# Performance work log

Measured on AMD Instinct MI355X. Metric: run time of the kernel, lower is better.

Reference implementation:

```python
import jax, jax.numpy as jnp
import numpy as np

D_MODEL = 512
NUM_HEADS = 8
HEAD_DIM = D_MODEL // NUM_HEADS  # 64
B, L = 8, 1024


def setup_inputs() -> dict:
    key = jax.random.key(0)
    ks = jax.random.split(key, 6)
    scale = 1.0 / np.sqrt(D_MODEL)
    return {
        "x": jax.random.normal(ks[0], (B, L, D_MODEL), dtype=jnp.float32),
        "mask": jax.random.normal(ks[1], (L, L), dtype=jnp.float32),
        "Wqkv": jax.random.normal(ks[2], (D_MODEL, 3 * D_MODEL), dtype=jnp.float32) * scale,
        "bqkv": jax.random.normal(ks[3], (3 * D_MODEL,), dtype=jnp.float32) * 0.01,
        "Wo": jax.random.normal(ks[4], (D_MODEL, D_MODEL), dtype=jnp.float32) * scale,
        "bo": jax.random.normal(ks[5], (D_MODEL,), dtype=jnp.float32) * 0.01,
    }


def reference(x, mask, Wqkv, bqkv, Wo, bo):
    b, l, _ = x.shape
    qkv = x @ Wqkv + bqkv                                   # [B, L, 3*D]
    # Faithful to torch: reshape to [B, L, H, 3*head_dim] then chunk last dim.
    qkv = qkv.reshape(b, l, NUM_HEADS, 3 * HEAD_DIM)
    qkv = jnp.transpose(qkv, (0, 2, 1, 3))                  # [B, H, L, 3*hd]
    q, k, v = jnp.split(qkv, 3, axis=-1)                    # each [B, H, L, hd]
    scaled = jnp.einsum("bhqd,bhkd->bhqk", q, k) / np.sqrt(HEAD_DIM)
    scaled = scaled + mask                                  # mask broadcasts over [B, H]
    attn = jax.nn.softmax(scaled, axis=-1)
    out = jnp.einsum("bhqk,bhkd->bhqd", attn, v)            # [B, H, L, hd]
    out = jnp.transpose(out, (0, 2, 1, 3)).reshape(b, l, D_MODEL)
    return out @ Wo + bo
```

## Files before the change

### kernel.cpp

```cpp
#include <hip/hip_runtime.h>
#include <hip/hip_bf16.h>
#include <stdint.h>

#define B_ 8
#define L_ 1024
#define DM 512
#define H_ 8
#define HD 64
#define N3 1536
#define M_T (B_*L_)
#define LOG2E 1.44269504f

typedef __attribute__((ext_vector_type(8))) short short8;
typedef __attribute__((ext_vector_type(4))) float f32x4;
typedef __attribute__((ext_vector_type(4))) float float4_t;
typedef __attribute__((ext_vector_type(4))) unsigned short ushort4_t;

#define MFMA16(a,b,c) __builtin_amdgcn_mfma_f32_16x16x32_bf16((a),(b),(c),0,0,0)

__device__ __forceinline__ short f2bf(float f){
  union { float f; unsigned u; } v; v.f = f;
  unsigned r = v.u + 0x7fffu + ((v.u >> 16) & 1u);
  return (short)(r >> 16);
}

__device__ __forceinline__ short f2bf_fast(float f){
  __hip_bfloat16 h = __float2bfloat16(f);
  short s; __builtin_memcpy(&s, &h, 2); return s;
}

__global__ __launch_bounds__(256) void k_cvt(const float* __restrict__ x,
                                             short* __restrict__ xb, int n8){
  int i = blockIdx.x*256 + threadIdx.x;
  if (i >= n8) return;
  const float4_t* p = (const float4_t*)x + (size_t)i*2;
  float4_t a = p[0], b = p[1];
  short8 o;
  o[0]=f2bf(a[0]); o[1]=f2bf(a[1]); o[2]=f2bf(a[2]); o[3]=f2bf(a[3]);
  o[4]=f2bf(b[0]); o[5]=f2bf(b[1]); o[6]=f2bf(b[2]); o[7]=f2bf(b[3]);
  *((short8*)xb + i) = o;
}

__global__ __launch_bounds__(256) void k_tr2(const float* __restrict__ W0, short* __restrict__ WT0,
                                             const float* __restrict__ W1, short* __restrict__ WT1){
  __shared__ float t[64][65];
  const float* W; short* WT; int N, n0;
  if (blockIdx.x < 24){ W = W0; WT = WT0; N = N3; n0 = blockIdx.x*64; }
  else                { W = W1; WT = WT1; N = DM; n0 = (blockIdx.x-24)*64; }
  int k0 = blockIdx.y*64;
  int tid = threadIdx.x;
  int r = tid >> 4, c4 = (tid & 15) * 4;
  #pragma unroll
  for (int it=0; it<4; ++it){
    int rr = r + it*16;
    float4_t v = *(const float4_t*)(W + (size_t)(k0+rr)*N + n0 + c4);
    t[rr][c4+0]=v[0]; t[rr][c4+1]=v[1]; t[rr][c4+2]=v[2]; t[rr][c4+3]=v[3];
  }
  __syncthreads();
  #pragma unroll
  for (int it=0; it<4; ++it){
    int n = r + it*16;
    ushort4_t o;
    o[0]=(unsigned short)f2bf(t[c4+0][n]);
    o[1]=(unsigned short)f2bf(t[c4+1][n]);
    o[2]=(unsigned short)f2bf(t[c4+2][n]);
    o[3]=(unsigned short)f2bf(t[c4+3][n]);
    *(ushort4_t*)(WT + (size_t)(n0+n)*DM + k0 + c4) = o;
  }
}

__global__ __launch_bounds__(256) void k_maskp(const float* __restrict__ mask,
                                               float* __restrict__ maskP){
  int gid = blockIdx.x*256 + threadIdx.x;
  int nf  = gid & 3;
  int lane= (gid>>2) & 63;
  int kvt = (gid>>8) & 15;
  int qg  = gid>>12;
  int li = lane & 15, lg = lane >> 4;
  int r0 = qg*16 + lg*4;
  int col = kvt*64 + nf*16 + li;
  float4_t o;
  #pragma unroll
  for (int j=0;j<4;++j)
    o[j] = fmaf(mask[(size_t)(r0+j)*1024 + col], LOG2E, -17.3123405f);
  ((float4_t*)maskP)[gid] = o;
}

__global__ __launch_bounds__(256) void k_gemm_qkv(
    const short* __restrict__ A, const short* __restrict__ Bt,
    const float* __restrict__ bias,
    short* __restrict__ Qo, short* __restrict__ Ko, short* __restrict__ VTo)
{
  __shared__ __align__(16) short As[2][128*40];
  __shared__ __align__(16) short Bs[2][128*40];
  const int m0 = blockIdx.x*128, n0 = blockIdx.y*128;
  const int tid = threadIdx.x;
  const int w = tid>>6, lane = tid&63, li = lane&15, lg = lane>>4;
  const int wr = (w>>1)*64, wc = (w&1)*64;

  int row[2], seg[2];
  #pragma unroll
  for (int c=0;c<2;++c){ int s = tid + c*256; row[c]=s>>2; seg[c]=s&3; }

  short8 ga[2], gb[2];
  #pragma unroll
  for (int c=0;c<2;++c){
    ga[c] = *(const short8*)(A  + (size_t)(m0+row[c])*DM + seg[c]*8);
    gb[c] = *(const short8*)(Bt + (size_t)(n0+row[c])*DM + seg[c]*8);
  }

  const f32x4 fz = {0.f,0.f,0.f,0.f};
  f32x4 acc[4][4];
  #pragma unroll
  for (int i=0;i<4;++i)
    #pragma unroll
    for (int j=0;j<4;++j) acc[i][j] = fz;

  for (int kt=0; kt<16; ++kt){
    short* as = As[kt&1]; short* bs = Bs[kt&1];
    #pragma unroll
    for (int c=0;c<2;++c){
      *(short8*)&as[row[c]*40 + seg[c]*8] = ga[c];
      *(short8*)&bs[row[c]*40 + seg[c]*8] = gb[c];
    }
    __syncthreads();
    if (kt < 15){
      int k0 = (kt+1)*32;
      #pragma unroll
      for (int c=0;c<2;++c){
        ga[c] = *(const short8*)(A  + (size_t)(m0+row[c])*DM + k0 + seg[c]*8);
        gb[c] = *(const short8*)(Bt + (size_t)(n0+row[c])*DM + k0 + seg[c]*8);
      }
    }
    short8 bfr[4];
    #pragma unroll
    for (int nf=0;nf<4;++nf)
      bfr[nf] = *(const short8*)&bs[(wc + nf*16 + li)*40 + lg*8];
    __builtin_amdgcn_s_setprio(1);
    #pragma unroll
    for (int mf=0;mf<4;++mf){
      short8 af = *(const short8*)&as[(wr + mf*16 + li)*40 + lg*8];
      #pragma unroll
      for (int nf=0;nf<4;++nf)
        acc[mf][nf] = MFMA16(af, bfr[nf], acc[mf][nf]);
    }
    __builtin_amdgcn_s_setprio(0);
    __syncthreads();
  }

  #pragma unroll
  for (int nf=0;nf<4;++nf){
    int n = n0 + wc + nf*16 + li;
    float bv = bias[n];
    unsigned h  = (unsigned)n / 192u;
    unsigned wn = (unsigned)n % 192u;
    unsigned typ = wn >> 6, d = wn & 63u;
    #pragma unroll
    for (int mf=0;mf<4;++mf){
      #pragma unroll
      for (int j=0;j<4;++j){
        int m  = m0 + wr + mf*16 + lg*4 + j;
        int b  = m >> 10, lp = m & 1023;
        size_t bh = (size_t)(b*8 + (int)h);
        float vf = acc[mf][nf][j] + bv;
        if (typ == 0)      Qo [(bh<<16) + ((size_t)lp<<6)  + d]  = f2bf_fast(vf * 0.18033688f);
        else if (typ == 1) Ko [(bh<<16) + ((size_t)lp<<6)  + d]  = f2bf_fast(vf);
        else               VTo[(bh<<16) + ((size_t)d<<10)  + lp] = f2bf_fast(vf);
      }
    }
  }
}

__global__ __launch_bounds__(512) void k_attn(
    const short* __restrict__ Q, const short* __restrict__ Kb,
    const short* __restrict__ VT, const float* __restrict__ maskP,
    short* __restrict__ O2)
{
  __shared__ __align__(16) short Ks[2][64*72];
  __shared__ __align__(16) short Vs[2][64*72];
  __shared__ __align__(16) short Ps[8][16*72];
  const int bh = blockIdx.y;
  const int q0 = blockIdx.x*128;
  const int tid = threadIdx.x, w = tid>>6, lane = tid&63, li = lane&15, lg = lane>>4;
  const int qw = q0 + w*16;

  const short* Qp = Q  + ((size_t)bh<<16);
  const short* Kp = Kb + ((size_t)bh<<16);
  const short* Vp = VT + ((size_t)bh<<16);

  short8 qf[2];
  #pragma unroll
  for (int t=0;t<2;++t)
    qf[t] = *(const short8*)(Qp + ((size_t)(qw+li)<<6) + t*32 + lg*8);

  short8 ones8;
  #pragma unroll
  for (int e=0;e<8;++e) ones8[e] = (short)0x3f80;

  const f32x4 fz = {0.f,0.f,0.f,0.f};
  f32x4 o[4], osum = fz;
  #pragma unroll
  for (int df=0;df<4;++df) o[df] = fz;

  const int srow = tid>>3, sseg8 = (tid&7)*8;

  short8 gk = *(const short8*)(Kp + ((size_t)srow<<6) + sseg8);
  short8 gv = *(const short8*)(Vp + ((size_t)srow<<10) + sseg8);
  *(short8*)&Ks[0][srow*72 + sseg8] = gk;
  *(short8*)&Vs[0][srow*72 + sseg8] = gv;
  gk = *(const short8*)(Kp + ((size_t)(64+srow)<<6) + sseg8);
  gv = *(const short8*)(Vp + ((size_t)srow<<10) + 64 + sseg8);
  __syncthreads();

  const float* mp0 = maskP + ((size_t)(qw>>4)<<14) + lane*16;
  short* pw = Ps[w];

  for (int kvt=0; kvt<16; ++kvt){
    const short* ks = Ks[kvt&1];
    const short* vs = Vs[kvt&1];
    if (kvt < 15){
      short* kd = Ks[(kvt&1)^1]; short* vd = Vs[(kvt&1)^1];
      *(short8*)&kd[srow*72 + sseg8] = gk;
      *(short8*)&vd[srow*72 + sseg8] = gv;
    }
    if (kvt < 14){
      int nx = (kvt+2)*64;
      gk = *(const short8*)(Kp + ((size_t)(nx+srow)<<6) + sseg8);
      gv = *(const short8*)(Vp + ((size_t)srow<<10) + nx + sseg8);
    }

    const float* mp = mp0 + (size_t)kvt*1024;
    f32x4 s[4];
    #pragma unroll
    for (int nf=0;nf<4;++nf)
      s[nf] = *(const float4_t*)(mp + nf*4);

    __builtin_amdgcn_s_setprio(1);
    #pragma unroll
    for (int nf=0;nf<4;++nf){
      #pragma unroll
      for (int t=0;t<2;++t){
        short8 kf = *(const short8*)&ks[(nf*16+li)*72 + t*32 + lg*8];
        s[nf] = MFMA16(qf[t], kf, s[nf]);
      }
    }
    __builtin_amdgcn_s_setprio(0);

    #pragma unroll
    for (int nf=0;nf<4;++nf)
      #pragma unroll
      for (int j=0;j<4;++j)
        pw[(lg*4+j)*72 + nf*16 + li] = f2bf_fast(exp2f(s[nf][j]));

    __builtin_amdgcn_s_setprio(1);
    #pragma unroll
    for (int t=0;t<2;++t){
      short8 pf = *(const short8*)&pw[li*72 + t*32 + lg*8];
      osum = MFMA16(pf, ones8, osum);
      #pragma unroll
      for (int df=0;df<4;++df){
        short8 vf = *(const short8*)&vs[(df*16+li)*72 + t*32 + lg*8];
        o[df] = MFMA16(pf, vf, o[df]);
      }
    }
    __builtin_amdgcn_s_setprio(0);

    __syncthreads();
  }

  int b = bh >> 3, h = bh & 7;
  float rl[4];
  #pragma unroll
  for (int j=0;j<4;++j) rl[j] = 1.0f / osum[j];
  #pragma unroll
  for (int df=0;df<4;++df)
    #pragma unroll
    for (int j=0;j<4;++j){
      int m   = b*1024 + qw + lg*4 + j;
      int col = h*64 + df*16 + li;
      O2[(size_t)m*512 + col] = f2bf_fast(o[df][j] * rl[j]);
    }
}

__global__ __launch_bounds__(256) void k_gemm_out(
    const short* __restrict__ A, const short* __restrict__ Bt,
    const float* __restrict__ bias, float* __restrict__ out)
{
  __shared__ __align__(16) short As[2][128*40];
  __shared__ __align__(16) short Bs[2][128*40];
  const int m0 = blockIdx.x*128, n0 = blockIdx.y*128;
  const int tid = threadIdx.x;
  const int w = tid>>6, lane = tid&63, li = lane&15, lg = lane>>4;
  const int wr = (w>>1)*64, wc = (w&1)*64;

  int row[2], seg[2];
  #pragma unroll
  for (int c=0;c<2;++c){ int s = tid + c*256; row[c]=s>>2; seg[c]=s&3; }

  short8 ga[2], gb[2];
  #pragma unroll
  for (int c=0;c<2;++c){
    ga[c] = *(const short8*)(A  + (size_t)(m0+row[c])*DM + seg[c]*8);
    gb[c] = *(const short8*)(Bt + (size_t)(n0+row[c])*DM + seg[c]*8);
  }

  const f32x4 fz = {0.f,0.f,0.f,0.f};
  f32x4 acc[4][4];
  #pragma unroll
  for (int i=0;i<4;++i)
    #pragma unroll
    for (int j=0;j<4;++j) acc[i][j] = fz;

  for (int kt=0; kt<16; ++kt){
    short* as = As[kt&1]; short* bs = Bs[kt&1];
    #pragma unroll
    for (int c=0;c<2;++c){
      *(short8*)&as[row[c]*40 + seg[c]*8] = ga[c];
      *(short8*)&bs[row[c]*40 + seg[c]*8] = gb[c];
    }
    __syncthreads();
    if (kt < 15){
      int k0 = (kt+1)*32;
      #pragma unroll
      for (int c=0;c<2;++c){
        ga[c] = *(const short8*)(A  + (size_t)(m0+row[c])*DM + k0 + seg[c]*8);
        gb[c] = *(const short8*)(Bt + (size_t)(n0+row[c])*DM + k0 + seg[c]*8);
      }
    }
    short8 bfr[4];
    #pragma unroll
    for (int nf=0;nf<4;++nf)
      bfr[nf] = *(const short8*)&bs[(wc + nf*16 + li)*40 + lg*8];
    __builtin_amdgcn_s_setprio(1);
    #pragma unroll
    for (int mf=0;mf<4;++mf){
      short8 af = *(const short8*)&as[(wr + mf*16 + li)*40 + lg*8];
      #pragma unroll
      for (int nf=0;nf<4;++nf)
        acc[mf][nf] = MFMA16(af, bfr[nf], acc[mf][nf]);
    }
    __builtin_amdgcn_s_setprio(0);
    __syncthreads();
  }

  #pragma unroll
  for (int nf=0;nf<4;++nf){
    int n = n0 + wc + nf*16 + li;
    float bv = bias[n];
    #pragma unroll
    for (int mf=0;mf<4;++mf){
      #pragma unroll
      for (int j=0;j<4;++j){
        int m = m0 + wr + mf*16 + lg*4 + j;
        out[(size_t)m*DM + n] = acc[mf][nf][j] + bv;
      }
    }
  }
}

extern "C" void kernel_launch(void* const* d_in, const int* in_sizes, int n_in,
                              void* d_out, int out_size, void* d_ws, size_t ws_size,
                              hipStream_t stream)
{
  (void)in_sizes; (void)n_in; (void)out_size; (void)ws_size;
  const float* x    = (const float*)d_in[0];
  const float* mask = (const float*)d_in[1];
  const float* Wqkv = (const float*)d_in[2];
  const float* bqkv = (const float*)d_in[3];
  const float* Wo   = (const float*)d_in[4];
  const float* bo   = (const float*)d_in[5];
  float* out = (float*)d_out;

  short* xb    = (short*)d_ws;
  short* WqkvT = xb    + (size_t)M_T*DM;
  short* WoT   = WqkvT + (size_t)N3*DM;
  short* Qb    = WoT   + (size_t)DM*DM;
  short* Kbf   = Qb    + (size_t)64*1024*64;
  short* VTb   = Kbf   + (size_t)64*1024*64;
  short* O2    = VTb   + (size_t)64*1024*64;
  float* maskP = (float*)xb;

  k_cvt<<<2048, 256, 0, stream>>>(x, xb, (M_T*DM)/8);
  k_tr2<<<dim3(32, 8), 256, 0, stream>>>(Wqkv, WqkvT, Wo, WoT);
  k_gemm_qkv<<<dim3(M_T/128, N3/128), 256, 0, stream>>>(xb, WqkvT, bqkv, Qb, Kbf, VTb);
  k_maskp<<<1024, 256, 0, stream>>>(mask, maskP);
  k_attn    <<<dim3(L_/128, B_*H_),   512, 0, stream>>>(Qb, Kbf, VTb, maskP, O2);
  k_gemm_out<<<dim3(M_T/128, DM/128), 256, 0, stream>>>(O2, WoT, bo, out);
}
```

Baseline: 93.76 us.

## Give each attention wave two query row-blocks, transpose score layout, prefetch mask

The attention kernel drops from 512 to 256 threads per block, and each wave now handles 32 query rows instead of 16. Each K and V fragment read from shared memory then feeds twice as many MFMAs. The QK^T product is computed transposed (K as the A operand), so the mask permutation and the P stores change layout, and P is packed with v_cvt_pk_bf16_f32 into wider stores. The next tile's mask is prefetched into registers, and the accumulator is seeded directly with the mask. The cost is higher register pressure and fewer waves per block, which could limit latency hiding.

```diff
diff --git a/kernel.cpp b/kernel.cpp
--- a/kernel.cpp
+++ b/kernel.cpp
@@ -15,6 +15,7 @@
 typedef __attribute__((ext_vector_type(4))) float f32x4;
 typedef __attribute__((ext_vector_type(4))) float float4_t;
 typedef __attribute__((ext_vector_type(4))) unsigned short ushort4_t;
+typedef __attribute__((ext_vector_type(2))) unsigned int u32x2;
 
 #define MFMA16(a,b,c) __builtin_amdgcn_mfma_f32_16x16x32_bf16((a),(b),(c),0,0,0)
 
@@ -77,12 +78,12 @@
   int kvt = (gid>>8) & 15;
   int qg  = gid>>12;
   int li = lane & 15, lg = lane >> 4;
-  int r0 = qg*16 + lg*4;
-  int col = kvt*64 + nf*16 + li;
+  int row = qg*16 + li;
+  int col = kvt*64 + nf*16 + lg*4;
+  float4_t m = *(const float4_t*)(mask + (size_t)row*1024 + col);
   float4_t o;
   #pragma unroll
-  for (int j=0;j<4;++j)
-    o[j] = fmaf(mask[(size_t)(r0+j)*1024 + col], LOG2E, -17.3123405f);
+  for (int j=0;j<4;++j) o[j] = fmaf(m[j], LOG2E, -17.3123405f);
   ((float4_t*)maskP)[gid] = o;
 }
 
@@ -171,48 +172,77 @@
   }
 }
 
-__global__ __launch_bounds__(512) void k_attn(
+__global__ __launch_bounds__(256, 2) void k_attn(
     const short* __restrict__ Q, const short* __restrict__ Kb,
     const short* __restrict__ VT, const float* __restrict__ maskP,
     short* __restrict__ O2)
 {
   __shared__ __align__(16) short Ks[2][64*72];
   __shared__ __align__(16) short Vs[2][64*72];
-  __shared__ __align__(16) short Ps[8][16*72];
+  __shared__ __align__(16) short Ps[4][32*72];
   const int bh = blockIdx.y;
   const int q0 = blockIdx.x*128;
   const int tid = threadIdx.x, w = tid>>6, lane = tid&63, li = lane&15, lg = lane>>4;
-  const int qw = q0 + w*16;
+  const int qw = q0 + w*32;
 
   const short* Qp = Q  + ((size_t)bh<<16);
   const short* Kp = Kb + ((size_t)bh<<16);
   const short* Vp = VT + ((size_t)bh<<16);
 
-  short8 qf[2];
-  #pragma unroll
-  for (int t=0;t<2;++t)
-    qf[t] = *(const short8*)(Qp + ((size_t)(qw+li)<<6) + t*32 + lg*8);
+  short8 qf[2][2];
+  #pragma unroll
+  for (int mb=0;mb<2;++mb)
+    #pragma unroll
+    for (int t=0;t<2;++t)
+      qf[mb][t] = *(const short8*)(Qp + ((size_t)(qw+mb*16+li)<<6) + t*32 + lg*8);
 
   short8 ones8;
   #pragma unroll
   for (int e=0;e<8;++e) ones8[e] = (short)0x3f80;
 
   const f32x4 fz = {0.f,0.f,0.f,0.f};
-  f32x4 o[4], osum = fz;
-  #pragma unroll
-  for (int df=0;df<4;++df) o[df] = fz;
-
-  const int srow = tid>>3, sseg8 = (tid&7)*8;
-
-  short8 gk = *(const short8*)(Kp + ((size_t)srow<<6) + sseg8);
-  short8 gv = *(const short8*)(Vp + ((size_t)srow<<10) + sseg8);
-  *(short8*)&Ks[0][srow*72 + sseg8] = gk;
-  *(short8*)&Vs[0][srow*72 + sseg8] = gv;
-  gk = *(const short8*)(Kp + ((size_t)(64+srow)<<6) + sseg8);
-  gv = *(const short8*)(Vp + ((size_t)srow<<10) + 64 + sseg8);
+  f32x4 o[2][4], osum[2];
+  #pragma unroll
+  for (int mb=0;mb<2;++mb){
+    osum[mb] = fz;
+    #pragma unroll
+    for (int df=0;df<4;++df) o[mb][df] = fz;
+  }
+
+  int srow[2], sseg[2];
+  #pragma unroll
+  for (int c=0;c<2;++c){ int f = tid + c*256; srow[c]=f>>3; sseg[c]=(f&7)*8; }
+
+  short8 gk[2], gv[2];
+  #pragma unroll
+  for (int c=0;c<2;++c){
+    gk[c] = *(const short8*)(Kp + ((size_t)srow[c]<<6)  + sseg[c]);
+    gv[c] = *(const short8*)(Vp + ((size_t)srow[c]<<10) + sseg[c]);
+  }
+  #pragma unroll
+  for (int c=0;c<2;++c){
+    *(short8*)&Ks[0][srow[c]*72 + sseg[c]] = gk[c];
+    *(short8*)&Vs[0][srow[c]*72 + sseg[c]] = gv[c];
+  }
+  #pragma unroll
+  for (int c=0;c<2;++c){
+    gk[c] = *(const short8*)(Kp + ((size_t)(64+srow[c])<<6) + sseg[c]);
+    gv[c] = *(const short8*)(Vp + ((size_t)srow[c]<<10) + 64 + sseg[c]);
+  }
+
+  const float* mpb[2];
+  #pragma unroll
+  for (int mb=0;mb<2;++mb)
+    mpb[mb] = maskP + ((size_t)((qw>>4)+mb)<<14) + lane*16;
+  f32x4 mnx[2][4];
+  #pragma unroll
+  for (int mb=0;mb<2;++mb)
+    #pragma unroll
+    for (int nf=0;nf<4;++nf)
+      mnx[mb][nf] = *(const float4_t*)(mpb[mb] + nf*4);
+
   __syncthreads();
 
-  const float* mp0 = maskP + ((size_t)(qw>>4)<<14) + lane*16;
   short* pw = Ps[w];
 
   for (int kvt=0; kvt<16; ++kvt){
@@ -220,47 +250,69 @@
     const short* vs = Vs[kvt&1];
     if (kvt < 15){
       short* kd = Ks[(kvt&1)^1]; short* vd = Vs[(kvt&1)^1];
-      *(short8*)&kd[srow*72 + sseg8] = gk;
-      *(short8*)&vd[srow*72 + sseg8] = gv;
+      #pragma unroll
+      for (int c=0;c<2;++c){
+        *(short8*)&kd[srow[c]*72 + sseg[c]] = gk[c];
+        *(short8*)&vd[srow[c]*72 + sseg[c]] = gv[c];
+      }
     }
     if (kvt < 14){
       int nx = (kvt+2)*64;
-      gk = *(const short8*)(Kp + ((size_t)(nx+srow)<<6) + sseg8);
-      gv = *(const short8*)(Vp + ((size_t)srow<<10) + nx + sseg8);
-    }
-
-    const float* mp = mp0 + (size_t)kvt*1024;
-    f32x4 s[4];
-    #pragma unroll
-    for (int nf=0;nf<4;++nf)
-      s[nf] = *(const float4_t*)(mp + nf*4);
-
+      #pragma unroll
+      for (int c=0;c<2;++c){
+        gk[c] = *(const short8*)(Kp + ((size_t)(nx+srow[c])<<6) + sseg[c]);
+        gv[c] = *(const short8*)(Vp + ((size_t)srow[c]<<10) + nx + sseg[c]);
+      }
+    }
+
+    f32x4 s[2][4];
     __builtin_amdgcn_s_setprio(1);
     #pragma unroll
     for (int nf=0;nf<4;++nf){
-      #pragma unroll
-      for (int t=0;t<2;++t){
-        short8 kf = *(const short8*)&ks[(nf*16+li)*72 + t*32 + lg*8];
-        s[nf] = MFMA16(qf[t], kf, s[nf]);
+      short8 kf0 = *(const short8*)&ks[(nf*16+li)*72 + lg*8];
+      short8 kf1 = *(const short8*)&ks[(nf*16+li)*72 + 32 + lg*8];
+      #pragma unroll
+      for (int mb=0;mb<2;++mb){
+        s[mb][nf] = MFMA16(kf0, qf[mb][0], mnx[mb][nf]);
+        s[mb][nf] = MFMA16(kf1, qf[mb][1], s[mb][nf]);
       }
     }
     __builtin_amdgcn_s_setprio(0);
 
-    #pragma unroll
-    for (int nf=0;nf<4;++nf)
-      #pragma unroll
-      for (int j=0;j<4;++j)
-        pw[(lg*4+j)*72 + nf*16 + li] = f2bf_fast(exp2f(s[nf][j]));
+    if (kvt < 15){
+      #pragma unroll
+      for (int mb=0;mb<2;++mb)
+        #pragma unroll
+        for (int nf=0;nf<4;++nf)
+          mnx[mb][nf] = *(const float4_t*)(mpb[mb] + (kvt+1)*1024 + nf*4);
+    }
+
+    #pragma unroll
+    for (int mb=0;mb<2;++mb){
+      #pragma unroll
+      for (int nf=0;nf<4;++nf){
+        float e0 = exp2f(s[mb][nf][0]), e1 = exp2f(s[mb][nf][1]);
+        float e2 = exp2f(s[mb][nf][2]), e3 = exp2f(s[mb][nf][3]);
+        unsigned p01, p23;
+        asm("v_cvt_pk_bf16_f32 %0, %1, %2" : "=v"(p01) : "v"(e0), "v"(e1));
+        asm("v_cvt_pk_bf16_f32 %0, %1, %2" : "=v"(p23) : "v"(e2), "v"(e3));
+        u32x2 pv; pv[0]=p01; pv[1]=p23;
+        *(u32x2*)&pw[(mb*16+li)*72 + nf*16 + lg*4] = pv;
+      }
+    }
 
     __builtin_amdgcn_s_setprio(1);
     #pragma unroll
     for (int t=0;t<2;++t){
-      short8 pf = *(const short8*)&pw[li*72 + t*32 + lg*8];
-      osum = MFMA16(pf, ones8, osum);
+      short8 pf0 = *(const short8*)&pw[(   li)*72 + t*32 + lg*8];
+      short8 pf1 = *(const short8*)&pw[(16+li)*72 + t*32 + lg*8];
+      osum[0] = MFMA16(pf0, ones8, osum[0]);
+      osum[1] = MFMA16(pf1, ones8, osum[1]);
       #pragma unroll
       for (int df=0;df<4;++df){
         short8 vf = *(const short8*)&vs[(df*16+li)*72 + t*32 + lg*8];
-        o[df] = MFMA16(pf, vf, o[df]);
+        o[0][df] = MFMA16(pf0, vf, o[0][df]);
+        o[1][df] = MFMA16(pf1, vf, o[1][df]);
       }
     }
     __builtin_amdgcn_s_setprio(0);
@@ -269,17 +321,20 @@
   }
 
   int b = bh >> 3, h = bh & 7;
-  float rl[4];
-  #pragma unroll
-  for (int j=0;j<4;++j) rl[j] = 1.0f / osum[j];
-  #pragma unroll
-  for (int df=0;df<4;++df)
-    #pragma unroll
-    for (int j=0;j<4;++j){
-      int m   = b*1024 + qw + lg*4 + j;
-      int col = h*64 + df*16 + li;
-      O2[(size_t)m*512 + col] = f2bf_fast(o[df][j] * rl[j]);
-    }
+  #pragma unroll
+  for (int mb=0;mb<2;++mb){
+    float rl[4];
+    #pragma unroll
+    for (int j=0;j<4;++j) rl[j] = 1.0f / osum[mb][j];
+    #pragma unroll
+    for (int df=0;df<4;++df)
+      #pragma unroll
+      for (int j=0;j<4;++j){
+        int m   = b*1024 + qw + mb*16 + lg*4 + j;
+        int col = h*64 + df*16 + li;
+        O2[(size_t)m*512 + col] = f2bf_fast(o[mb][df][j] * rl[j]);
+      }
+  }
 }
 
 __global__ __launch_bounds__(256) void k_gemm_out(
@@ -384,6 +439,6 @@
   k_tr2<<<dim3(32, 8), 256, 0, stream>>>(Wqkv, WqkvT, Wo, WoT);
   k_gemm_qkv<<<dim3(M_T/128, N3/128), 256, 0, stream>>>(xb, WqkvT, bqkv, Qb, Kbf, VTb);
   k_maskp<<<1024, 256, 0, stream>>>(mask, maskP);
-  k_attn    <<<dim3(L_/128, B_*H_),   512, 0, stream>>>(Qb, Kbf, VTb, maskP, O2);
+  k_attn    <<<dim3(L_/128, B_*H_),   256, 0, stream>>>(Qb, Kbf, VTb, maskP, O2);
   k_gemm_out<<<dim3(M_T/128, DM/128), 256, 0, stream>>>(O2, WoT, bo, out);
 }
```

After: 89.86 us. -4.2%, faster.
